# Optimization experiments

Measured on AMD Instinct MI355X. Metric: run time of the kernel, lower is better.

Reference implementation:

```python
import jax, jax.numpy as jnp
import numpy as np

EPS = 1e-8

@jax.custom_vjp
def spike(x):
    # Heaviside forward, SuperSpike surrogate gradient in backward
    return (x > 0.0).astype(x.dtype)

def _spike_fwd(x):
    return spike(x), x

def _spike_bwd(x, g):
    return (g / (1.0 + 10.0 * jnp.abs(x)) ** 2,)

spike.defvjp(_spike_fwd, _spike_bwd)


def setup_inputs() -> dict:
    key = jax.random.key(0)
    k1, k2, k3, k4 = jax.random.split(key, 4)
    B, T, I, O = 128, 128, 1024, 1024
    x = jax.random.normal(k1, (B, T, I), dtype=jnp.float32)
    # w ~ N(0, 1/sqrt(I)) per reset_parameters
    w = jax.random.normal(k2, (I, O), dtype=jnp.float32) * np.float32(1.0 / np.sqrt(I))
    # beta ~ N(0.7, 0.01), clamped to [0,1]
    beta = jnp.clip(0.7 + 0.01 * jax.random.normal(k3, (1,), dtype=jnp.float32), 0.0, 1.0)
    # b ~ N(1.0, 0.01), clamped to >= 0
    b = jnp.clip(1.0 + 0.01 * jax.random.normal(k4, (1024,), dtype=jnp.float32), 0.0, None)
    return {"x": x, "w": w, "beta": beta, "b": b}


def reference(x, w, beta, b):
    # x: [B, T, I]; w: [I, O]; beta: [1]; b: [O]
    h = jnp.einsum('btc,cd->btd', x, w)                 # [B, T, O]
    d = jnp.einsum('ab,ac->bc', w, w)                    # lateral reset matrix [O, O]
    norm = (w ** 2).sum(0)                               # [O]
    inv_norm = 1.0 / (norm + EPS)
    B, O = x.shape[0], w.shape[1]

    def step(carry, h_t):
        mem, spk = carry
        rst = spk @ d                                    # [B, O]
        mem = (mem - rst) * beta + h_t * (1.0 - beta)
        mthr = mem * inv_norm - b
        spk = spike(mthr)
        return (mem, spk), spk

    init = (jnp.zeros((B, O), x.dtype), jnp.zeros((B, O), x.dtype))
    _, spk_rec = jax.lax.scan(step, init, jnp.swapaxes(h, 0, 1))  # [T, B, O]
    spk_rec = jnp.swapaxes(spk_rec, 0, 1)                # [B, T, O]
    loss = 0.5 * (spk_rec ** 2).mean()
    return spk_rec, loss
```

## Files before the change

kernel.cpp:

```cpp
#include <hip/hip_runtime.h>
#include <hip/hip_fp16.h>

#define B_ 128
#define T_ 128
#define I_ 1024
#define O_ 1024
#define M_ (B_*T_)
#define NOUT (M_*O_)

typedef __attribute__((ext_vector_type(8))) _Float16 half8;
typedef __attribute__((ext_vector_type(4))) float floatx4;

__device__ __forceinline__ void gld_lds16(const void* g, void* l) {
    __builtin_amdgcn_global_load_lds((const __attribute__((address_space(1))) void*)g,
                                     (__attribute__((address_space(3))) void*)l,
                                     16, 0, 0);
}

__device__ __forceinline__ void barrier_lds_only() {
    asm volatile("" ::: "memory");
    __builtin_amdgcn_s_waitcnt(0xC07F);
    __builtin_amdgcn_s_barrier();
    asm volatile("" ::: "memory");
}

__device__ __forceinline__ void split3h(float x, unsigned short& h,
                                        unsigned short& m, unsigned short& l) {
    __half f0 = __float2half(x);
    float r1 = x - __half2float(f0);
    __half f1 = __float2half(r1);
    float r2 = r1 - __half2float(f1);
    __half f2 = __float2half(r2);
    h = __half_as_ushort(f0);
    m = __half_as_ushort(f1);
    l = __half_as_ushort(f2);
}

__global__ __launch_bounds__(256) void split_x(const float* __restrict__ X,
                                               unsigned short* __restrict__ Xh,
                                               unsigned short* __restrict__ Xm,
                                               unsigned short* __restrict__ Xl) {
    size_t base = ((size_t)blockIdx.x * 256 + threadIdx.x) * 4;
    float4 v = *(const float4*)(X + base);
    ushort4 hh, mm, ll;
    split3h(v.x, hh.x, mm.x, ll.x);
    split3h(v.y, hh.y, mm.y, ll.y);
    split3h(v.z, hh.z, mm.z, ll.z);
    split3h(v.w, hh.w, mm.w, ll.w);
    *(ushort4*)(Xh + base) = hh;
    *(ushort4*)(Xm + base) = mm;
    *(ushort4*)(Xl + base) = ll;
}

__global__ __launch_bounds__(256) void split_wt(const float* __restrict__ W,
                                                unsigned short* __restrict__ WTh,
                                                unsigned short* __restrict__ WTm,
                                                unsigned short* __restrict__ WTl) {
    __shared__ float t[64][65];
    const int tid = threadIdx.x;
    const int tx = tid & 63, ty4 = tid >> 6;
    const int r0 = blockIdx.x * 64, c0 = blockIdx.y * 64;
#pragma unroll
    for (int j = 0; j < 16; ++j) {
        int row = j * 4 + ty4;
        t[row][tx] = W[(size_t)(r0 + row) * O_ + c0 + tx];
    }
    __syncthreads();
#pragma unroll
    for (int j = 0; j < 16; ++j) {
        int i = j * 4 + ty4;
        float v = t[tx][i];
        unsigned short h, m, l;
        split3h(v, h, m, l);
        size_t off = (size_t)(c0 + i) * I_ + r0 + tx;
        WTh[off] = h; WTm[off] = m; WTl[off] = l;
    }
}

__global__ __launch_bounds__(512, 2) void gemm_h_mfma(
        const unsigned short* __restrict__ Xh, const unsigned short* __restrict__ Xm,
        const unsigned short* __restrict__ Xl, const unsigned short* __restrict__ WTh,
        const unsigned short* __restrict__ WTm, const unsigned short* __restrict__ WTl,
        float* __restrict__ H) {
    const int K = I_, N = O_;
    __shared__ unsigned short P[2][36864];

    const int tid = threadIdx.x;
    const int lane = tid & 63;
    const int wid = tid >> 6;
    const int wrow = wid >> 2;
    const int wcol = wid & 3;
    const int l15 = lane & 15, quad = lane >> 4;
    const int bm = blockIdx.x * 128, bn = blockIdx.y * 256;

    const int srow = tid >> 2, sch = tid & 3;
    const int schg = sch ^ ((srow >> 1) & 3);
    const unsigned short* gsrcA[3];
    const unsigned short* gsrcB[3];
    gsrcA[0] = Xh  + (size_t)(bm + srow) * K + schg * 8;
    gsrcA[1] = Xm  + (size_t)(bm + srow) * K + schg * 8;
    gsrcA[2] = Xl  + (size_t)(bm + srow) * K + schg * 8;
    gsrcB[0] = WTh + (size_t)(bn + srow) * K + schg * 8;
    gsrcB[1] = WTm + (size_t)(bn + srow) * K + schg * 8;
    gsrcB[2] = WTl + (size_t)(bn + srow) * K + schg * 8;

    auto stage = [&](int kt) {
        unsigned short* wb = &P[0][0] + (size_t)(kt & 1) * 36864;
        const size_t k0 = (size_t)kt * 32;
#pragma unroll
        for (int p = 0; p < 3; ++p)
            gld_lds16(gsrcA[p] + k0, wb + p * 4096 + tid * 8);
#pragma unroll
        for (int p = 0; p < 3; ++p) {
            unsigned short* bb = wb + 12288 + p * 8192 + tid * 8;
            gld_lds16(gsrcB[p] + k0, bb);
            gld_lds16(gsrcB[p] + (size_t)128 * K + k0, bb + 4096);
        }
    };

    floatx4 acc[4][4];
#pragma unroll
    for (int mt = 0; mt < 4; ++mt)
#pragma unroll
        for (int nt = 0; nt < 4; ++nt) acc[mt][nt] = (floatx4)(0.f);

    stage(0);

    for (int kt = 0; kt < 32; ++kt) {
        const unsigned short* rb = &P[0][0] + (size_t)(kt & 1) * 36864;

        asm volatile("" ::: "memory");
        __builtin_amdgcn_s_waitcnt(0x1F70);
        __builtin_amdgcn_s_barrier();
        asm volatile("" ::: "memory");

        half8 Af[3][4];
#pragma unroll
        for (int pa = 0; pa < 3; ++pa)
#pragma unroll
            for (int mt = 0; mt < 4; ++mt) {
                const int row = wrow * 64 + mt * 16 + l15;
                const int chk = quad ^ ((row >> 1) & 3);
                Af[pa][mt] = *(const half8*)(rb + pa * 4096 + row * 32 + chk * 8);
            }

        if (kt < 31) stage(kt + 1);

#pragma unroll
        for (int pb = 0; pb < 3; ++pb) {
            half8 Bf[4];
#pragma unroll
            for (int nt = 0; nt < 4; ++nt) {
                const int col = wcol * 64 + nt * 16 + l15;
                const int chk = quad ^ ((col >> 1) & 3);
                Bf[nt] = *(const half8*)(rb + 12288 + pb * 8192 + col * 32 + chk * 8);
            }
#pragma unroll
            for (int nt = 0; nt < 4; ++nt)
#pragma unroll
                for (int mt = 0; mt < 4; ++mt) {
                    acc[mt][nt] = __builtin_amdgcn_mfma_f32_16x16x32_f16(Af[0][mt], Bf[nt], acc[mt][nt], 0, 0, 0);
                    if (pb < 2)
                        acc[mt][nt] = __builtin_amdgcn_mfma_f32_16x16x32_f16(Af[1][mt], Bf[nt], acc[mt][nt], 0, 0, 0);
                    if (pb == 0)
                        acc[mt][nt] = __builtin_amdgcn_mfma_f32_16x16x32_f16(Af[2][mt], Bf[nt], acc[mt][nt], 0, 0, 0);
                }
        }
    }

#pragma unroll
    for (int mt = 0; mt < 4; ++mt)
#pragma unroll
        for (int nt = 0; nt < 4; ++nt) {
            int grow = bm + wrow * 64 + mt * 16 + quad * 4;
            int gcol = bn + wcol * 64 + nt * 16 + l15;
            float* hp = H + (size_t)grow * N + gcol;
#pragma unroll
            for (int r = 0; r < 4; ++r) hp[(size_t)r * N] = acc[mt][nt][r];
        }
}

__global__ void colnorm_diag(const float* __restrict__ D, float* __restrict__ invn,
                             unsigned int* __restrict__ counter) {
    int o = blockIdx.x * 256 + threadIdx.x;
    if (o == 0) *counter = 0u;
    invn[o] = 1.0f / (D[(size_t)o * O_ + o] + 1e-8f);
}

__global__ __launch_bounds__(512) void scan_kernel(const float* __restrict__ h,
                                                   const float* __restrict__ d,
                                                   const float* __restrict__ invn,
                                                   const float* __restrict__ bias,
                                                   const float* __restrict__ beta,
                                                   float* __restrict__ out,
                                                   unsigned int* __restrict__ spike_count) {
    __shared__ int lst[2][O_];
    __shared__ int cnt[T_ + 1];
    __shared__ unsigned int red[512];

    const int tid = threadIdx.x;
    const int lane = tid & 63;
    const int b = blockIdx.x;
    const int o2 = tid * 2;
    const float betav = beta[0];
    const float omb = 1.0f - betav;

    const float2 invn2 = *(const float2*)(invn + o2);
    const float2 b2 = *(const float2*)(bias + o2);
    float2 mem2 = make_float2(0.f, 0.f);

    for (int i = tid; i <= T_; i += 512) cnt[i] = 0;
    unsigned int local_count = 0;
    const float* hb = h + (size_t)b * T_ * O_;
    float* ob = out + (size_t)b * T_ * O_;
    const unsigned long long below = (lane == 63) ? 0xFFFFFFFFFFFFFFFFull >> 1
                                                  : ((1ull << lane) - 1ull);

    float2 hcur = *(const float2*)(hb + o2);
    __syncthreads();

    for (int t = 0; t < T_; ++t) {
        const int p = t & 1, q = p ^ 1;
        const int n = cnt[t];

        float2 hnext = make_float2(0.f, 0.f);
        if (t + 1 < T_) hnext = *(const float2*)(hb + (size_t)(t + 1) * O_ + o2);

        float2 rst = make_float2(0.f, 0.f);
        int i = 0;
        for (; i + 16 <= n; i += 16) {
            float2 v[16];
#pragma unroll
            for (int u = 0; u < 16; ++u) {
                const int j = lst[p][i + u];
                v[u] = *(const float2*)(d + (size_t)j * O_ + o2);
            }
#pragma unroll
            for (int u = 0; u < 16; ++u) { rst.x += v[u].x; rst.y += v[u].y; }
        }
        for (; i + 4 <= n; i += 4) {
            float2 v[4];
#pragma unroll
            for (int u = 0; u < 4; ++u) {
                const int j = lst[p][i + u];
                v[u] = *(const float2*)(d + (size_t)j * O_ + o2);
            }
#pragma unroll
            for (int u = 0; u < 4; ++u) { rst.x += v[u].x; rst.y += v[u].y; }
        }
        for (; i < n; ++i) {
            const int j = lst[p][i];
            float2 v = *(const float2*)(d + (size_t)j * O_ + o2);
            rst.x += v.x; rst.y += v.y;
        }

        mem2.x = (mem2.x - rst.x) * betav + hcur.x * omb;
        mem2.y = (mem2.y - rst.y) * betav + hcur.y * omb;

        const int s0 = (mem2.x * invn2.x - b2.x) > 0.0f;
        const int s1 = (mem2.y * invn2.y - b2.y) > 0.0f;

        float2 sv = make_float2(s0 ? 1.f : 0.f, s1 ? 1.f : 0.f);
        *(float2*)(ob + (size_t)t * O_ + o2) = sv;
        local_count += (unsigned)(s0 + s1);

        unsigned long long mk0 = __ballot(s0);
        unsigned long long mk1 = __ballot(s1);
        const int c0 = __popcll(mk0);
        const int tot = c0 + __popcll(mk1);
        int base = 0;
        if (lane == 0 && tot) base = atomicAdd(&cnt[t + 1], tot);
        base = __shfl(base, 0, 64);
        if (s0) lst[q][base + __popcll(mk0 & below)] = o2 + 0;
        base += c0;
        if (s1) lst[q][base + __popcll(mk1 & below)] = o2 + 1;

        barrier_lds_only();
        hcur = hnext;
    }

    red[tid] = local_count;
    __syncthreads();
    for (int st = 256; st > 0; st >>= 1) {
        if (tid < st) red[tid] += red[tid + st];
        __syncthreads();
    }
    if (tid == 0) atomicAdd(spike_count, red[0]);
}

__global__ void finalize_loss(const unsigned int* __restrict__ spike_count,
                              float* __restrict__ loss_out) {
    *loss_out = 0.5f * ((float)(*spike_count) / 16777216.0f);
}

extern "C" void kernel_launch(void* const* d_in, const int* in_sizes, int n_in,
                              void* d_out, int out_size, void* d_ws, size_t ws_size,
                              hipStream_t stream) {
    const float* x    = (const float*)d_in[0];
    const float* w    = (const float*)d_in[1];
    const float* beta = (const float*)d_in[2];
    const float* bias = (const float*)d_in[3];
    float* out = (float*)d_out;

    char* ws = (char*)d_ws;
    float* h    = (float*)ws;
    float* dmat = (float*)(ws + (size_t)67108864);
    float* invn = (float*)(ws + (size_t)71303168);
    unsigned int* cntp = (unsigned int*)(ws + (size_t)71307264);
    unsigned short* wt_h = (unsigned short*)(ws + (size_t)71311360);
    unsigned short* wt_m = (unsigned short*)(ws + (size_t)73408512);
    unsigned short* wt_l = (unsigned short*)(ws + (size_t)75505664);
    unsigned short* x_h  = (unsigned short*)(ws + (size_t)77602816);
    unsigned short* x_m  = (unsigned short*)(ws + (size_t)111157248);
    unsigned short* x_l  = (unsigned short*)(ws + (size_t)144711680);

    split_x<<<M_ * I_ / 1024, 256, 0, stream>>>(x, x_h, x_m, x_l);
    split_wt<<<dim3(I_ / 64, O_ / 64), 256, 0, stream>>>(w, wt_h, wt_m, wt_l);
    gemm_h_mfma<<<dim3(M_ / 128, O_ / 256), 512, 0, stream>>>(x_h, x_m, x_l,
                                                              wt_h, wt_m, wt_l, h);
    gemm_h_mfma<<<dim3(O_ / 128, O_ / 256), 512, 0, stream>>>(wt_h, wt_m, wt_l,
                                                              wt_h, wt_m, wt_l, dmat);
    colnorm_diag<<<O_ / 256, 256, 0, stream>>>(dmat, invn, cntp);
    scan_kernel<<<B_, 512, 0, stream>>>(h, dmat, invn, bias, beta, out, cntp);
    finalize_loss<<<1, 1, 0, stream>>>(cntp, out + (size_t)NOUT);
}
```

Measured before the change: 478.8 us.

## Use 32x32x16 MFMA tiles in split-fp16 GEMM and compute WᵀW in fp32

Switches the main split-precision GEMM from 16x16x32 MFMA tiles to 32x32x16 tiles, with 2x2 accumulators per wave and a matching LDS fragment load and output store pattern. The aim is fewer LDS fragment reads per MFMA and higher MFMA throughput. Separately, the lateral reset matrix WᵀW is now computed by a plain fp32 SIMT tiled kernel rather than the split-fp16 MFMA GEMM. That gives exact fp32 products for the reset matrix and norms, but the small GEMM now runs on the slower vector ALUs.

```diff
diff --git a/kernel.cpp b/kernel.cpp
--- a/kernel.cpp
+++ b/kernel.cpp
@@ -9,7 +9,7 @@
 #define NOUT (M_*O_)
 
 typedef __attribute__((ext_vector_type(8))) _Float16 half8;
-typedef __attribute__((ext_vector_type(4))) float floatx4;
+typedef __attribute__((ext_vector_type(16))) float floatx16;
 
 __device__ __forceinline__ void gld_lds16(const void* g, void* l) {
     __builtin_amdgcn_global_load_lds((const __attribute__((address_space(1))) void*)g,
@@ -90,7 +90,8 @@
     const int wid = tid >> 6;
     const int wrow = wid >> 2;
     const int wcol = wid & 3;
-    const int l15 = lane & 15, quad = lane >> 4;
+    const int l31 = lane & 31;
+    const int khalf = lane >> 5;
     const int bm = blockIdx.x * 128, bn = blockIdx.y * 256;
 
     const int srow = tid >> 2, sch = tid & 3;
@@ -118,11 +119,11 @@
         }
     };
 
-    floatx4 acc[4][4];
-#pragma unroll
-    for (int mt = 0; mt < 4; ++mt)
-#pragma unroll
-        for (int nt = 0; nt < 4; ++nt) acc[mt][nt] = (floatx4)(0.f);
+    floatx16 acc[2][2];
+#pragma unroll
+    for (int mt = 0; mt < 2; ++mt)
+#pragma unroll
+        for (int nt = 0; nt < 2; ++nt) acc[mt][nt] = (floatx16)(0.f);
 
     stage(0);
 
@@ -134,50 +135,106 @@
         __builtin_amdgcn_s_barrier();
         asm volatile("" ::: "memory");
 
-        half8 Af[3][4];
+        half8 Af[3][2][2];
 #pragma unroll
         for (int pa = 0; pa < 3; ++pa)
 #pragma unroll
-            for (int mt = 0; mt < 4; ++mt) {
-                const int row = wrow * 64 + mt * 16 + l15;
-                const int chk = quad ^ ((row >> 1) & 3);
-                Af[pa][mt] = *(const half8*)(rb + pa * 4096 + row * 32 + chk * 8);
+            for (int mt = 0; mt < 2; ++mt) {
+                const int row = wrow * 64 + mt * 32 + l31;
+                const int sw = (row >> 1) & 3;
+#pragma unroll
+                for (int ks = 0; ks < 2; ++ks) {
+                    const int chk = (ks * 2 + khalf) ^ sw;
+                    Af[pa][mt][ks] = *(const half8*)(rb + pa * 4096 + row * 32 + chk * 8);
+                }
             }
 
         if (kt < 31) stage(kt + 1);
 
 #pragma unroll
         for (int pb = 0; pb < 3; ++pb) {
-            half8 Bf[4];
-#pragma unroll
-            for (int nt = 0; nt < 4; ++nt) {
-                const int col = wcol * 64 + nt * 16 + l15;
-                const int chk = quad ^ ((col >> 1) & 3);
-                Bf[nt] = *(const half8*)(rb + 12288 + pb * 8192 + col * 32 + chk * 8);
-            }
-#pragma unroll
-            for (int nt = 0; nt < 4; ++nt)
-#pragma unroll
-                for (int mt = 0; mt < 4; ++mt) {
-                    acc[mt][nt] = __builtin_amdgcn_mfma_f32_16x16x32_f16(Af[0][mt], Bf[nt], acc[mt][nt], 0, 0, 0);
-                    if (pb < 2)
-                        acc[mt][nt] = __builtin_amdgcn_mfma_f32_16x16x32_f16(Af[1][mt], Bf[nt], acc[mt][nt], 0, 0, 0);
-                    if (pb == 0)
-                        acc[mt][nt] = __builtin_amdgcn_mfma_f32_16x16x32_f16(Af[2][mt], Bf[nt], acc[mt][nt], 0, 0, 0);
+            half8 Bf[2][2];
+#pragma unroll
+            for (int nt = 0; nt < 2; ++nt) {
+                const int col = wcol * 64 + nt * 32 + l31;
+                const int sw = (col >> 1) & 3;
+#pragma unroll
+                for (int ks = 0; ks < 2; ++ks) {
+                    const int chk = (ks * 2 + khalf) ^ sw;
+                    Bf[nt][ks] = *(const half8*)(rb + 12288 + pb * 8192 + col * 32 + chk * 8);
                 }
-        }
-    }
-
-#pragma unroll
-    for (int mt = 0; mt < 4; ++mt)
-#pragma unroll
-        for (int nt = 0; nt < 4; ++nt) {
-            int grow = bm + wrow * 64 + mt * 16 + quad * 4;
-            int gcol = bn + wcol * 64 + nt * 16 + l15;
-            float* hp = H + (size_t)grow * N + gcol;
-#pragma unroll
-            for (int r = 0; r < 4; ++r) hp[(size_t)r * N] = acc[mt][nt][r];
-        }
+            }
+#pragma unroll
+            for (int nt = 0; nt < 2; ++nt)
+#pragma unroll
+                for (int mt = 0; mt < 2; ++mt)
+#pragma unroll
+                    for (int ks = 0; ks < 2; ++ks) {
+                        acc[mt][nt] = __builtin_amdgcn_mfma_f32_32x32x16_f16(Af[0][mt][ks], Bf[nt][ks], acc[mt][nt], 0, 0, 0);
+                        if (pb < 2)
+                            acc[mt][nt] = __builtin_amdgcn_mfma_f32_32x32x16_f16(Af[1][mt][ks], Bf[nt][ks], acc[mt][nt], 0, 0, 0);
+                        if (pb == 0)
+                            acc[mt][nt] = __builtin_amdgcn_mfma_f32_32x32x16_f16(Af[2][mt][ks], Bf[nt][ks], acc[mt][nt], 0, 0, 0);
+                    }
+        }
+    }
+
+#pragma unroll
+    for (int mt = 0; mt < 2; ++mt)
+#pragma unroll
+        for (int nt = 0; nt < 2; ++nt) {
+            const int gcol = bn + wcol * 64 + nt * 32 + l31;
+#pragma unroll
+            for (int r = 0; r < 16; ++r) {
+                const int grow = bm + wrow * 64 + mt * 32 + (r & 3) + 8 * (r >> 2) + 4 * khalf;
+                H[(size_t)grow * N + gcol] = acc[mt][nt][r];
+            }
+        }
+}
+
+__global__ __launch_bounds__(256) void gemm_wtw(const float* __restrict__ W,
+                                                float* __restrict__ D) {
+    const int K = I_, N = O_;
+    __shared__ float As[32][68];
+    __shared__ float Bs[32][68];
+    const int tid = threadIdx.x;
+    const int tx = tid & 15, ty = tid >> 4;
+    const int bj = blockIdx.x * 64, bo = blockIdx.y * 64;
+    const int lr = tid >> 4;
+    const int lc = (tid & 15) << 2;
+
+    float acc[4][4];
+#pragma unroll
+    for (int m = 0; m < 4; m++)
+#pragma unroll
+        for (int n = 0; n < 4; n++) acc[m][n] = 0.f;
+
+    for (int k0 = 0; k0 < K; k0 += 32) {
+        float4 a0 = *(const float4*)(W + (size_t)(k0 + lr) * N + bj + lc);
+        float4 a1 = *(const float4*)(W + (size_t)(k0 + lr + 16) * N + bj + lc);
+        float4 b0 = *(const float4*)(W + (size_t)(k0 + lr) * N + bo + lc);
+        float4 b1 = *(const float4*)(W + (size_t)(k0 + lr + 16) * N + bo + lc);
+        __syncthreads();
+        *(float4*)&As[lr][lc] = a0; *(float4*)&As[lr + 16][lc] = a1;
+        *(float4*)&Bs[lr][lc] = b0; *(float4*)&Bs[lr + 16][lc] = b1;
+        __syncthreads();
+#pragma unroll
+        for (int k = 0; k < 32; ++k) {
+            float4 av = *(const float4*)&As[k][ty * 4];
+            float4 bv = *(const float4*)&Bs[k][tx * 4];
+            float am[4] = {av.x, av.y, av.z, av.w};
+            float bb[4] = {bv.x, bv.y, bv.z, bv.w};
+#pragma unroll
+            for (int m = 0; m < 4; m++)
+#pragma unroll
+                for (int n = 0; n < 4; n++) acc[m][n] += am[m] * bb[n];
+        }
+    }
+#pragma unroll
+    for (int m = 0; m < 4; m++) {
+        float4 v = make_float4(acc[m][0], acc[m][1], acc[m][2], acc[m][3]);
+        *(float4*)(D + (size_t)(bj + ty * 4 + m) * N + bo + tx * 4) = v;
+    }
 }
 
 __global__ void colnorm_diag(const float* __restrict__ D, float* __restrict__ invn,
@@ -318,8 +375,7 @@
     split_wt<<<dim3(I_ / 64, O_ / 64), 256, 0, stream>>>(w, wt_h, wt_m, wt_l);
     gemm_h_mfma<<<dim3(M_ / 128, O_ / 256), 512, 0, stream>>>(x_h, x_m, x_l,
                                                               wt_h, wt_m, wt_l, h);
-    gemm_h_mfma<<<dim3(O_ / 128, O_ / 256), 512, 0, stream>>>(wt_h, wt_m, wt_l,
-                                                              wt_h, wt_m, wt_l, dmat);
+    gemm_wtw<<<dim3(O_ / 64, O_ / 64), 256, 0, stream>>>(w, dmat);
     colnorm_diag<<<O_ / 256, 256, 0, stream>>>(dmat, invn, cntp);
     scan_kernel<<<B_, 512, 0, stream>>>(h, dmat, invn, bias, beta, out, cntp);
     finalize_loss<<<1, 1, 0, stream>>>(cntp, out + (size_t)NOUT);
```

Result: slower. 490.8 us (+2.5%).
